# Optimization experiments

Hardware: AMD Instinct MI355X
Metric: run time of the kernel (lower is better)

## Reference

```python
import jax, jax.numpy as jnp
import numpy as np

EPS = 1e-06

def setup_inputs() -> dict:
    key = jax.random.key(0)
    k1, k2, k3 = jax.random.split(key, 3)
    N, L, H, D = 4, 4096, 16, 64
    return {
        "queries": jax.random.normal(k1, (N, L, H, D), dtype=jnp.float32),
        "keys": jax.random.normal(k2, (N, L, H, D), dtype=jnp.float32),
        "values": jax.random.normal(k3, (N, L, H, D), dtype=jnp.float32),
    }

def reference(queries, keys, values):
    # [N, L, H, D] -> [N, H, L, D]
    q = jnp.transpose(queries, (0, 2, 1, 3))
    k = jnp.transpose(keys, (0, 2, 1, 3))
    v = jnp.transpose(values, (0, 2, 1, 3))
    # kernel feature map
    q = jax.nn.sigmoid(q)
    k = jax.nn.sigmoid(k)
    L = q.shape[2]
    S = k.shape[2]
    # incoming/outgoing flow normalizers
    normalizer_row = 1.0 / jnp.einsum('nhld,nhd->nhl', q + EPS, k.sum(axis=2) + EPS)
    normalizer_col = 1.0 / jnp.einsum('nhsd,nhd->nhs', k + EPS, q.sum(axis=2) + EPS)
    # refined normalizers (competition / allocation)
    row_refine = jnp.einsum('nhld,nhd->nhl', q + EPS,
                            (k * normalizer_col[..., None]).sum(axis=2) + EPS)
    col_refine = jnp.einsum('nhsd,nhd->nhs', k + EPS,
                            (q * normalizer_row[..., None]).sum(axis=2) + EPS)
    row_refine = jax.nn.sigmoid(row_refine * (float(L) / float(S)))
    col_refine = jax.nn.softmax(col_refine, axis=-1) * S
    # linear attention aggregation: kv is [N, H, D, D]
    kv = jnp.einsum('nhsd,nhse->nhde', k, v * col_refine[..., None])
    x = jnp.einsum('nhld,nhde->nhle', q, kv) * (normalizer_row * row_refine)[..., None]
    # back to [N, L, H, D]
    return jnp.transpose(x, (0, 2, 1, 3))
```

## Files before the change

kernel.cpp:

```cpp
#include <hip/hip_runtime.h>
#include <math.h>

#define EPS 1e-6f
constexpr int N_ = 4, L_ = 4096, H_ = 16, D_ = 64;
constexpr int NH = N_ * H_;
constexpr int HD = H_ * D_;
constexpr long NSTRIDE = (long)L_ * HD;
constexpr int KCHUNKS = 16;

typedef __attribute__((ext_vector_type(8))) short short8;
typedef __attribute__((ext_vector_type(4))) float f32x4;

__device__ float g_qsum[NH * D_];
__device__ float g_ksum[NH * D_];
__device__ float g_qnr[NH * D_];
__device__ float g_knc[NH * D_];
__device__ float g_nr[NH * L_];
__device__ float g_coefrow[NH * L_];
__device__ float g_cr[NH * L_];
__device__ int   g_smax[NH];
__device__ float g_ssum[NH];
__device__ float g_kv[NH * D_ * D_];
__device__ float g_kvpart[KCHUNKS * NH * D_ * D_];

__device__ __forceinline__ float sigm(float x) {
    return 1.0f / (1.0f + __expf(-x));
}
__device__ __forceinline__ float4 sigm4(float4 x) {
    float4 r;
    r.x = sigm(x.x); r.y = sigm(x.y); r.z = sigm(x.z); r.w = sigm(x.w);
    return r;
}
__device__ __forceinline__ unsigned rne_hi(unsigned xb) {
    return (xb + 0x7fffu + ((xb >> 16) & 1u)) & 0xffff0000u;
}
__device__ __forceinline__ uint2 pack_split3(float x) {
    unsigned xb = __float_as_uint(x);
    unsigned h1 = rne_hi(xb);
    float r1 = x - __uint_as_float(h1);
    unsigned h2 = rne_hi(__float_as_uint(r1));
    float r2 = r1 - __uint_as_float(h2);
    unsigned h3 = rne_hi(__float_as_uint(r2));
    uint2 o;
    o.x = h1 | (h2 >> 16);
    o.y = h3 >> 16;
    return o;
}

__global__ void k0_zero() {
    int i = blockIdx.x * blockDim.x + threadIdx.x;
    int st = gridDim.x * blockDim.x;
    for (int j = i; j < NH * D_; j += st) {
        g_qsum[j] = 0.f; g_ksum[j] = 0.f; g_qnr[j] = 0.f; g_knc[j] = 0.f;
    }
    for (int j = i; j < NH; j += st) { g_smax[j] = 0; g_ssum[j] = 0.f; }
}

__global__ __launch_bounds__(256) void k1_sums(const float* __restrict__ q,
                                               const float* __restrict__ k) {
    int nh = blockIdx.y, n = nh >> 4, h = nh & 15;
    const float* src = blockIdx.z ? k : q;
    float* dst = blockIdx.z ? g_ksum : g_qsum;
    int t = threadIdx.x, c4 = t & 15, rg = t >> 4;
    long nbase = (long)n * NSTRIDE + (long)h * D_ + c4 * 4;
    int l0 = blockIdx.x * 128;
    float4 a = make_float4(0.f, 0.f, 0.f, 0.f);
#pragma unroll
    for (int j = 0; j < 8; ++j) {
        int r = rg + j * 16;
        float4 x = *(const float4*)&src[nbase + (long)(l0 + r) * HD];
        float4 s = sigm4(x);
        a.x += s.x; a.y += s.y; a.z += s.z; a.w += s.w;
    }
    __shared__ float4 lds[256];
    lds[t] = a;
    __syncthreads();
    if (t < 16) {
        float4 s = make_float4(0.f, 0.f, 0.f, 0.f);
#pragma unroll
        for (int g = 0; g < 16; ++g) {
            float4 b = lds[t + g * 16];
            s.x += b.x; s.y += b.y; s.z += b.z; s.w += b.w;
        }
        atomicAdd(&dst[nh * 64 + t * 4 + 0], s.x);
        atomicAdd(&dst[nh * 64 + t * 4 + 1], s.y);
        atomicAdd(&dst[nh * 64 + t * 4 + 2], s.z);
        atomicAdd(&dst[nh * 64 + t * 4 + 3], s.w);
    }
}

__global__ __launch_bounds__(256) void k2_norm(const float* __restrict__ q,
                                               const float* __restrict__ k) {
    int nh = blockIdx.y, n = nh >> 4, h = nh & 15;
    bool colside = blockIdx.z != 0;
    const float* src = colside ? k : q;
    const float* sums = colside ? g_qsum : g_ksum;
    float* acc = colside ? g_knc : g_qnr;
    __shared__ float tile[128 * 64];
    __shared__ float bvec[64];
    __shared__ float nrl[128];
    __shared__ float part[256];
    int t = threadIdx.x;
    int l0 = blockIdx.x * 128;
    long nbase = (long)n * NSTRIDE + (long)h * D_;
    if (t < 64) bvec[t] = sums[nh * 64 + t] + EPS;
#pragma unroll
    for (int j = 0; j < 8; ++j) {
        int e_ = t + j * 256;
        int r = e_ >> 4, c4 = e_ & 15;
        float4 x = *(const float4*)&src[nbase + (long)(l0 + r) * HD + c4 * 4];
        *(float4*)&tile[r * 64 + c4 * 4] = sigm4(x);
    }
    __syncthreads();
    {
        int r = t & 127, h2 = t >> 7;
        float a = 0.f;
#pragma unroll
        for (int jj = 0; jj < 32; ++jj) {
            int j = (r + h2 * 32 + jj) & 63;
            a += (tile[r * 64 + j] + EPS) * bvec[j];
        }
        part[t] = a;
    }
    __syncthreads();
    if (t < 128) {
        float inv = 1.f / (part[t] + part[t + 128]);
        nrl[t] = inv;
        if (!colside) g_nr[nh * L_ + l0 + t] = inv;
    }
    __syncthreads();
    {
        int d = t & 63, rg = t >> 6;
        float a = 0.f;
#pragma unroll
        for (int rr = 0; rr < 32; ++rr) {
            int r = rg * 32 + rr;
            a += tile[r * 64 + d] * nrl[r];
        }
        part[t] = a;
    }
    __syncthreads();
    if (t < 64)
        atomicAdd(&acc[nh * 64 + t], part[t] + part[t + 64] + part[t + 128] + part[t + 192]);
}

__global__ __launch_bounds__(256) void k3_refine(const float* __restrict__ q,
                                                 const float* __restrict__ k) {
    int nh = blockIdx.y, n = nh >> 4, h = nh & 15;
    bool colside = blockIdx.z != 0;
    const float* src = colside ? k : q;
    const float* accv = colside ? g_qnr : g_knc;
    __shared__ float tile[128 * 64];
    __shared__ float bvec[64];
    __shared__ float part[256];
    __shared__ float pmax[128];
    int t = threadIdx.x;
    int l0 = blockIdx.x * 128;
    long nbase = (long)n * NSTRIDE + (long)h * D_;
    if (t < 64) bvec[t] = accv[nh * 64 + t] + EPS;
#pragma unroll
    for (int j = 0; j < 8; ++j) {
        int e_ = t + j * 256;
        int r = e_ >> 4, c4 = e_ & 15;
        float4 x = *(const float4*)&src[nbase + (long)(l0 + r) * HD + c4 * 4];
        *(float4*)&tile[r * 64 + c4 * 4] = sigm4(x);
    }
    __syncthreads();
    {
        int r = t & 127, h2 = t >> 7;
        float a = 0.f;
#pragma unroll
        for (int jj = 0; jj < 32; ++jj) {
            int j = (r + h2 * 32 + jj) & 63;
            a += (tile[r * 64 + j] + EPS) * bvec[j];
        }
        part[t] = a;
    }
    __syncthreads();
    if (t < 128) {
        float p = part[t] + part[t + 128];
        int l = l0 + t;
        if (!colside) {
            g_coefrow[nh * L_ + l] = g_nr[nh * L_ + l] * sigm(p);
        } else {
            g_cr[nh * L_ + l] = p;
            pmax[t] = p;
        }
    }
    __syncthreads();
    if (colside) {
        if (t < 64) pmax[t] = fmaxf(pmax[t], pmax[t + 64]);
        __syncthreads();
        if (t < 32) pmax[t] = fmaxf(pmax[t], pmax[t + 32]);
        __syncthreads();
        if (t == 0) {
            float m = pmax[0];
            for (int i = 1; i < 32; ++i) m = fmaxf(m, pmax[i]);
            atomicMax(&g_smax[nh], __float_as_int(m));
        }
    }
}

__global__ __launch_bounds__(256) void k3b_softmax() {
    int nh = blockIdx.y;
    int t = threadIdx.x;
    float mx = __int_as_float(g_smax[nh]);
    int base = nh * L_ + blockIdx.x * 1024;
    float local = 0.f;
    for (int j = t; j < 1024; j += 256) {
        float e = __expf(g_cr[base + j] - mx);
        g_cr[base + j] = e;
        local += e;
    }
    __shared__ float lds[256];
    lds[t] = local;
    __syncthreads();
    for (int s = 128; s; s >>= 1) {
        if (t < s) lds[t] += lds[t + s];
        __syncthreads();
    }
    if (t == 0) atomicAdd(&g_ssum[nh], lds[0]);
}

__global__ __launch_bounds__(256) void k4_kv(const float* __restrict__ k,
                                             const float* __restrict__ v) {
    int nh = blockIdx.y, n = nh >> 4, h = nh & 15;
    int t = threadIdx.x, lane = t & 63, wv = t >> 6;
    __shared__ uint2 ktile[32 * 67];
    __shared__ uint2 vtile[32 * 67];
    __shared__ float crs[256];
    float scale = (float)L_ / g_ssum[nh];
    int s0blk = blockIdx.x * 256;
    crs[t] = g_cr[nh * L_ + s0blk + t] * scale;

    f32x4 acc[4];
#pragma unroll
    for (int e = 0; e < 4; ++e) acc[e] = (f32x4){0.f, 0.f, 0.f, 0.f};

    long nbase = (long)n * NSTRIDE + (long)h * D_;
    int m = lane & 15, qd = lane >> 4;

    for (int sub = 0; sub < 8; ++sub) {
        int s0 = sub * 32;
        __syncthreads();
#pragma unroll
        for (int j = 0; j < 2; ++j) {
            int idx = t + j * 256;
            int r = idx >> 4, c4 = idx & 15;
            long gi = nbase + (long)(s0blk + s0 + r) * HD + c4 * 4;
            float4 kk = *(const float4*)&k[gi];
            float4 vv = *(const float4*)&v[gi];
            float c = crs[s0 + r];
            float4 ks4 = sigm4(kk);
            uint2 kp0 = pack_split3(ks4.x * c), kp1 = pack_split3(ks4.y * c);
            uint2 kp2 = pack_split3(ks4.z * c), kp3 = pack_split3(ks4.w * c);
            uint2 vp0 = pack_split3(vv.x), vp1 = pack_split3(vv.y);
            uint2 vp2 = pack_split3(vv.z), vp3 = pack_split3(vv.w);
            uint2* kdst = &ktile[r * 67 + c4 * 4];
            uint2* vdst = &vtile[r * 67 + c4 * 4];
            *(uint4*)&kdst[0] = make_uint4(kp0.x, kp0.y, kp1.x, kp1.y);
            *(uint4*)&kdst[2] = make_uint4(kp2.x, kp2.y, kp3.x, kp3.y);
            *(uint4*)&vdst[0] = make_uint4(vp0.x, vp0.y, vp1.x, vp1.y);
            *(uint4*)&vdst[2] = make_uint4(vp2.x, vp2.y, vp3.x, vp3.y);
        }
        __syncthreads();
        {
            short8 a1, a2, a3;
#pragma unroll
            for (int j = 0; j < 8; ++j) {
                uint2 aw = ktile[(qd * 8 + j) * 67 + wv * 16 + m];
                a1[j] = (short)(aw.x >> 16);
                a2[j] = (short)(aw.x & 0xffffu);
                a3[j] = (short)(aw.y);
            }
#pragma unroll
            for (int e = 0; e < 4; ++e) {
                short8 b1, b2, b3;
#pragma unroll
                for (int j = 0; j < 8; ++j) {
                    uint2 bw = vtile[(qd * 8 + j) * 67 + e * 16 + m];
                    b1[j] = (short)(bw.x >> 16);
                    b2[j] = (short)(bw.x & 0xffffu);
                    b3[j] = (short)(bw.y);
                }
                acc[e] = __builtin_amdgcn_mfma_f32_16x16x32_bf16(a1, b1, acc[e], 0, 0, 0);
                acc[e] = __builtin_amdgcn_mfma_f32_16x16x32_bf16(a1, b2, acc[e], 0, 0, 0);
                acc[e] = __builtin_amdgcn_mfma_f32_16x16x32_bf16(a2, b1, acc[e], 0, 0, 0);
                acc[e] = __builtin_amdgcn_mfma_f32_16x16x32_bf16(a1, b3, acc[e], 0, 0, 0);
                acc[e] = __builtin_amdgcn_mfma_f32_16x16x32_bf16(a3, b1, acc[e], 0, 0, 0);
                acc[e] = __builtin_amdgcn_mfma_f32_16x16x32_bf16(a2, b2, acc[e], 0, 0, 0);
            }
        }
    }
    float* dst = &g_kvpart[((long)blockIdx.x * NH + nh) * 4096];
#pragma unroll
    for (int e = 0; e < 4; ++e) {
#pragma unroll
        for (int r = 0; r < 4; ++r) {
            int d = wv * 16 + qd * 4 + r;
            int ec = e * 16 + m;
            dst[d * 64 + ec] = acc[e][r];
        }
    }
}

__global__ __launch_bounds__(256) void k4b_reduce() {
    int nh = blockIdx.x, t = threadIdx.x;
#pragma unroll
    for (int j = 0; j < 4; ++j) {
        int i4 = t + j * 256;
        float4 s = make_float4(0.f, 0.f, 0.f, 0.f);
        for (int c = 0; c < KCHUNKS; ++c) {
            float4 p = ((const float4*)&g_kvpart[((long)c * NH + nh) * 4096])[i4];
            s.x += p.x; s.y += p.y; s.z += p.z; s.w += p.w;
        }
        ((float4*)&g_kv[nh * 4096])[i4] = s;
    }
}

__global__ __launch_bounds__(256) void k5_out(const float* __restrict__ q,
                                              float* __restrict__ out) {
    int nh = blockIdx.y, n = nh >> 4, h = nh & 15;
    int t = threadIdx.x;
    __shared__ float kvt[64 * 64];
    __shared__ float qt[64][65];
#pragma unroll
    for (int j = 0; j < 4; j++)
        *(float4*)&kvt[(t + j * 256) * 4] = *(const float4*)&g_kv[nh * 4096 + (t + j * 256) * 4];
    int l0 = blockIdx.x * 64;
    long nbase = (long)n * NSTRIDE + (long)h * D_;
#pragma unroll
    for (int j = 0; j < 4; j++) {
        int e_ = t + j * 256;
        int r = e_ >> 4, c4 = e_ & 15;
        float4 x = *(const float4*)&q[nbase + (long)(l0 + r) * HD + c4 * 4];
        float4 s = sigm4(x);
        qt[r][c4 * 4 + 0] = s.x;
        qt[r][c4 * 4 + 1] = s.y;
        qt[r][c4 * 4 + 2] = s.z;
        qt[r][c4 * 4 + 3] = s.w;
    }
    __syncthreads();
    int e4 = t & 15, lg = t >> 4;
    float acc[4][4];
#pragma unroll
    for (int r = 0; r < 4; r++)
#pragma unroll
        for (int c = 0; c < 4; c++) acc[r][c] = 0.f;
#pragma unroll 8
    for (int d = 0; d < 64; ++d) {
        float4 kvv = *(const float4*)&kvt[d * 64 + e4 * 4];
#pragma unroll
        for (int r = 0; r < 4; r++) {
            float qv = qt[lg * 4 + r][d];
            acc[r][0] += qv * kvv.x;
            acc[r][1] += qv * kvv.y;
            acc[r][2] += qv * kvv.z;
            acc[r][3] += qv * kvv.w;
        }
    }
#pragma unroll
    for (int r = 0; r < 4; r++) {
        int l = l0 + lg * 4 + r;
        float coef = g_coefrow[nh * L_ + l];
        float4 o;
        o.x = acc[r][0] * coef;
        o.y = acc[r][1] * coef;
        o.z = acc[r][2] * coef;
        o.w = acc[r][3] * coef;
        *(float4*)&out[nbase + (long)l * HD + e4 * 4] = o;
    }
}

extern "C" void kernel_launch(void* const* d_in, const int* in_sizes, int n_in,
                              void* d_out, int out_size, void* d_ws, size_t ws_size,
                              hipStream_t stream) {
    const float* q = (const float*)d_in[0];
    const float* k = (const float*)d_in[1];
    const float* v = (const float*)d_in[2];
    float* out = (float*)d_out;

    k0_zero<<<64, 256, 0, stream>>>();
    k1_sums<<<dim3(L_ / 128, NH, 2), 256, 0, stream>>>(q, k);
    k2_norm<<<dim3(L_ / 128, NH, 2), 256, 0, stream>>>(q, k);
    k3_refine<<<dim3(L_ / 128, NH, 2), 256, 0, stream>>>(q, k);
    k3b_softmax<<<dim3(L_ / 1024, NH), 256, 0, stream>>>();
    k4_kv<<<dim3(KCHUNKS, NH), 256, 0, stream>>>(k, v);
    k4b_reduce<<<NH, 256, 0, stream>>>();
    k5_out<<<dim3(L_ / 64, NH), 256, 0, stream>>>(q, out);
}
```

Measured before the change: 334.7 us.

## Fuse refine and softmax into KV and output kernels, drop intermediate passes

Removes the separate refine and softmax kernels. The column-refine dot product and its exponential now run inside the KV-accumulation kernel, with the softmax sum collected by atomics and applied at the reduction step. The row-refine coefficient is computed on the fly in the output kernel. This cuts one full pass over q/k plus several per-row global buffers. The sum and normalizer kernels now process contiguous rows spanning all heads, using 16-lane shuffles instead of LDS reductions. The split-bf16 MFMA KV product is replaced with a plain fp32 FMA tile loop. The trade-offs are that softmax skips max subtraction, which risks overflow on other inputs, and that the KV matmul moves off the matrix cores.

```diff
diff --git a/kernel.cpp b/kernel.cpp
--- a/kernel.cpp
+++ b/kernel.cpp
@@ -6,22 +6,15 @@
 constexpr int NH = N_ * H_;
 constexpr int HD = H_ * D_;
 constexpr long NSTRIDE = (long)L_ * HD;
-constexpr int KCHUNKS = 16;
-
-typedef __attribute__((ext_vector_type(8))) short short8;
-typedef __attribute__((ext_vector_type(4))) float f32x4;
+constexpr int SCHUNKS = 32;
 
 __device__ float g_qsum[NH * D_];
 __device__ float g_ksum[NH * D_];
 __device__ float g_qnr[NH * D_];
 __device__ float g_knc[NH * D_];
-__device__ float g_nr[NH * L_];
-__device__ float g_coefrow[NH * L_];
-__device__ float g_cr[NH * L_];
-__device__ int   g_smax[NH];
 __device__ float g_ssum[NH];
 __device__ float g_kv[NH * D_ * D_];
-__device__ float g_kvpart[KCHUNKS * NH * D_ * D_];
+__device__ float g_kvpart[(long)SCHUNKS * NH * D_ * D_];
 
 __device__ __forceinline__ float sigm(float x) {
     return 1.0f / (1.0f + __expf(-x));
@@ -31,20 +24,12 @@
     r.x = sigm(x.x); r.y = sigm(x.y); r.z = sigm(x.z); r.w = sigm(x.w);
     return r;
 }
-__device__ __forceinline__ unsigned rne_hi(unsigned xb) {
-    return (xb + 0x7fffu + ((xb >> 16) & 1u)) & 0xffff0000u;
-}
-__device__ __forceinline__ uint2 pack_split3(float x) {
-    unsigned xb = __float_as_uint(x);
-    unsigned h1 = rne_hi(xb);
-    float r1 = x - __uint_as_float(h1);
-    unsigned h2 = rne_hi(__float_as_uint(r1));
-    float r2 = r1 - __uint_as_float(h2);
-    unsigned h3 = rne_hi(__float_as_uint(r2));
-    uint2 o;
-    o.x = h1 | (h2 >> 16);
-    o.y = h3 >> 16;
-    return o;
+__device__ __forceinline__ float red16(float p) {
+    p += __shfl_xor(p, 1);
+    p += __shfl_xor(p, 2);
+    p += __shfl_xor(p, 4);
+    p += __shfl_xor(p, 8);
+    return p;
 }
 
 __global__ void k0_zero() {
@@ -53,269 +38,156 @@
     for (int j = i; j < NH * D_; j += st) {
         g_qsum[j] = 0.f; g_ksum[j] = 0.f; g_qnr[j] = 0.f; g_knc[j] = 0.f;
     }
-    for (int j = i; j < NH; j += st) { g_smax[j] = 0; g_ssum[j] = 0.f; }
+    for (int j = i; j < NH; j += st) g_ssum[j] = 0.f;
 }
 
 __global__ __launch_bounds__(256) void k1_sums(const float* __restrict__ q,
                                                const float* __restrict__ k) {
-    int nh = blockIdx.y, n = nh >> 4, h = nh & 15;
     const float* src = blockIdx.z ? k : q;
     float* dst = blockIdx.z ? g_ksum : g_qsum;
-    int t = threadIdx.x, c4 = t & 15, rg = t >> 4;
-    long nbase = (long)n * NSTRIDE + (long)h * D_ + c4 * 4;
-    int l0 = blockIdx.x * 128;
-    float4 a = make_float4(0.f, 0.f, 0.f, 0.f);
-#pragma unroll
-    for (int j = 0; j < 8; ++j) {
-        int r = rg + j * 16;
-        float4 x = *(const float4*)&src[nbase + (long)(l0 + r) * HD];
+    int t = threadIdx.x;
+    long g0 = (long)blockIdx.x * 32;
+    int n = (int)(g0 >> 12);
+    const float* p = src + g0 * HD + t * 4;
+    float ax = 0.f, ay = 0.f, az = 0.f, aw = 0.f;
+#pragma unroll 8
+    for (int r = 0; r < 32; ++r) {
+        float4 x = *(const float4*)(p + (long)r * HD);
         float4 s = sigm4(x);
-        a.x += s.x; a.y += s.y; a.z += s.z; a.w += s.w;
-    }
-    __shared__ float4 lds[256];
-    lds[t] = a;
-    __syncthreads();
-    if (t < 16) {
-        float4 s = make_float4(0.f, 0.f, 0.f, 0.f);
-#pragma unroll
-        for (int g = 0; g < 16; ++g) {
-            float4 b = lds[t + g * 16];
-            s.x += b.x; s.y += b.y; s.z += b.z; s.w += b.w;
-        }
-        atomicAdd(&dst[nh * 64 + t * 4 + 0], s.x);
-        atomicAdd(&dst[nh * 64 + t * 4 + 1], s.y);
-        atomicAdd(&dst[nh * 64 + t * 4 + 2], s.z);
-        atomicAdd(&dst[nh * 64 + t * 4 + 3], s.w);
-    }
+        ax += s.x; ay += s.y; az += s.z; aw += s.w;
+    }
+    float* d0 = dst + n * 1024 + t * 4;
+    atomicAdd(d0 + 0, ax);
+    atomicAdd(d0 + 1, ay);
+    atomicAdd(d0 + 2, az);
+    atomicAdd(d0 + 3, aw);
 }
 
 __global__ __launch_bounds__(256) void k2_norm(const float* __restrict__ q,
                                                const float* __restrict__ k) {
-    int nh = blockIdx.y, n = nh >> 4, h = nh & 15;
-    bool colside = blockIdx.z != 0;
-    const float* src = colside ? k : q;
-    const float* sums = colside ? g_qsum : g_ksum;
-    float* acc = colside ? g_knc : g_qnr;
-    __shared__ float tile[128 * 64];
-    __shared__ float bvec[64];
-    __shared__ float nrl[128];
-    __shared__ float part[256];
-    int t = threadIdx.x;
-    int l0 = blockIdx.x * 128;
-    long nbase = (long)n * NSTRIDE + (long)h * D_;
-    if (t < 64) bvec[t] = sums[nh * 64 + t] + EPS;
-#pragma unroll
-    for (int j = 0; j < 8; ++j) {
-        int e_ = t + j * 256;
-        int r = e_ >> 4, c4 = e_ & 15;
-        float4 x = *(const float4*)&src[nbase + (long)(l0 + r) * HD + c4 * 4];
-        *(float4*)&tile[r * 64 + c4 * 4] = sigm4(x);
-    }
-    __syncthreads();
-    {
-        int r = t & 127, h2 = t >> 7;
-        float a = 0.f;
-#pragma unroll
-        for (int jj = 0; jj < 32; ++jj) {
-            int j = (r + h2 * 32 + jj) & 63;
-            a += (tile[r * 64 + j] + EPS) * bvec[j];
-        }
-        part[t] = a;
-    }
-    __syncthreads();
-    if (t < 128) {
-        float inv = 1.f / (part[t] + part[t + 128]);
-        nrl[t] = inv;
-        if (!colside) g_nr[nh * L_ + l0 + t] = inv;
-    }
-    __syncthreads();
-    {
-        int d = t & 63, rg = t >> 6;
-        float a = 0.f;
-#pragma unroll
-        for (int rr = 0; rr < 32; ++rr) {
-            int r = rg * 32 + rr;
-            a += tile[r * 64 + d] * nrl[r];
-        }
-        part[t] = a;
-    }
-    __syncthreads();
-    if (t < 64)
-        atomicAdd(&acc[nh * 64 + t], part[t] + part[t + 64] + part[t + 128] + part[t + 192]);
-}
-
-__global__ __launch_bounds__(256) void k3_refine(const float* __restrict__ q,
-                                                 const float* __restrict__ k) {
-    int nh = blockIdx.y, n = nh >> 4, h = nh & 15;
-    bool colside = blockIdx.z != 0;
-    const float* src = colside ? k : q;
-    const float* accv = colside ? g_qnr : g_knc;
-    __shared__ float tile[128 * 64];
-    __shared__ float bvec[64];
-    __shared__ float part[256];
-    __shared__ float pmax[128];
-    int t = threadIdx.x;
-    int l0 = blockIdx.x * 128;
-    long nbase = (long)n * NSTRIDE + (long)h * D_;
-    if (t < 64) bvec[t] = accv[nh * 64 + t] + EPS;
-#pragma unroll
-    for (int j = 0; j < 8; ++j) {
-        int e_ = t + j * 256;
-        int r = e_ >> 4, c4 = e_ & 15;
-        float4 x = *(const float4*)&src[nbase + (long)(l0 + r) * HD + c4 * 4];
-        *(float4*)&tile[r * 64 + c4 * 4] = sigm4(x);
-    }
-    __syncthreads();
-    {
-        int r = t & 127, h2 = t >> 7;
-        float a = 0.f;
-#pragma unroll
-        for (int jj = 0; jj < 32; ++jj) {
-            int j = (r + h2 * 32 + jj) & 63;
-            a += (tile[r * 64 + j] + EPS) * bvec[j];
-        }
-        part[t] = a;
-    }
-    __syncthreads();
-    if (t < 128) {
-        float p = part[t] + part[t + 128];
-        int l = l0 + t;
-        if (!colside) {
-            g_coefrow[nh * L_ + l] = g_nr[nh * L_ + l] * sigm(p);
-        } else {
-            g_cr[nh * L_ + l] = p;
-            pmax[t] = p;
-        }
-    }
-    __syncthreads();
-    if (colside) {
-        if (t < 64) pmax[t] = fmaxf(pmax[t], pmax[t + 64]);
-        __syncthreads();
-        if (t < 32) pmax[t] = fmaxf(pmax[t], pmax[t + 32]);
-        __syncthreads();
-        if (t == 0) {
-            float m = pmax[0];
-            for (int i = 1; i < 32; ++i) m = fmaxf(m, pmax[i]);
-            atomicMax(&g_smax[nh], __float_as_int(m));
-        }
-    }
-}
-
-__global__ __launch_bounds__(256) void k3b_softmax() {
-    int nh = blockIdx.y;
-    int t = threadIdx.x;
-    float mx = __int_as_float(g_smax[nh]);
-    int base = nh * L_ + blockIdx.x * 1024;
-    float local = 0.f;
-    for (int j = t; j < 1024; j += 256) {
-        float e = __expf(g_cr[base + j] - mx);
-        g_cr[base + j] = e;
-        local += e;
-    }
-    __shared__ float lds[256];
-    lds[t] = local;
-    __syncthreads();
-    for (int s = 128; s; s >>= 1) {
-        if (t < s) lds[t] += lds[t + s];
-        __syncthreads();
-    }
-    if (t == 0) atomicAdd(&g_ssum[nh], lds[0]);
-}
-
-__global__ __launch_bounds__(256) void k4_kv(const float* __restrict__ k,
+    bool col = blockIdx.z != 0;
+    const float* src = col ? k : q;
+    const float* sums = col ? g_qsum : g_ksum;
+    float* acc = col ? g_knc : g_qnr;
+    int t = threadIdx.x;
+    long g0 = (long)blockIdx.x * 32;
+    int n = (int)(g0 >> 12);
+    float4 bv = *(const float4*)(sums + n * 1024 + t * 4);
+    bv.x += EPS; bv.y += EPS; bv.z += EPS; bv.w += EPS;
+    const float* p = src + g0 * HD + t * 4;
+    float ax = 0.f, ay = 0.f, az = 0.f, aw = 0.f;
+#pragma unroll 4
+    for (int r = 0; r < 32; ++r) {
+        float4 x = *(const float4*)(p + (long)r * HD);
+        float4 s = sigm4(x);
+        float pd = (s.x + EPS) * bv.x + (s.y + EPS) * bv.y
+                 + (s.z + EPS) * bv.z + (s.w + EPS) * bv.w;
+        pd = red16(pd);
+        float inv = 1.0f / pd;
+        ax += s.x * inv; ay += s.y * inv; az += s.z * inv; aw += s.w * inv;
+    }
+    float* d0 = acc + n * 1024 + t * 4;
+    atomicAdd(d0 + 0, ax);
+    atomicAdd(d0 + 1, ay);
+    atomicAdd(d0 + 2, az);
+    atomicAdd(d0 + 3, aw);
+}
+
+__global__ __launch_bounds__(256) void k3_kv(const float* __restrict__ k,
                                              const float* __restrict__ v) {
     int nh = blockIdx.y, n = nh >> 4, h = nh & 15;
-    int t = threadIdx.x, lane = t & 63, wv = t >> 6;
-    __shared__ uint2 ktile[32 * 67];
-    __shared__ uint2 vtile[32 * 67];
-    __shared__ float crs[256];
+    int t = threadIdx.x;
+    __shared__ float ktile[128 * 64];
+    __shared__ float vtile[128 * 64];
+    __shared__ float pbuf[128];
+    __shared__ float redb[128];
+    __shared__ float qnrbuf[64];
+    if (t < 16) {
+        float4 w = *(const float4*)&g_qnr[nh * 64 + t * 4];
+        w.x += EPS; w.y += EPS; w.z += EPS; w.w += EPS;
+        *(float4*)&qnrbuf[t * 4] = w;
+    }
+    __syncthreads();
+    int rb = t >> 4, c4 = t & 15;
+    float4 qn = *(const float4*)&qnrbuf[c4 * 4];
+    long nbase = (long)n * NSTRIDE + (long)h * D_;
+    int s0 = blockIdx.x * 128;
+#pragma unroll
+    for (int j = 0; j < 8; ++j) {
+        int r = rb + j * 16;
+        long gi = nbase + (long)(s0 + r) * HD + c4 * 4;
+        float4 kk = *(const float4*)&k[gi];
+        float4 vv = *(const float4*)&v[gi];
+        float4 sk = sigm4(kk);
+        *(float4*)&ktile[r * 64 + c4 * 4] = sk;
+        *(float4*)&vtile[r * 64 + c4 * 4] = vv;
+        float pd = (sk.x + EPS) * qn.x + (sk.y + EPS) * qn.y
+                 + (sk.z + EPS) * qn.z + (sk.w + EPS) * qn.w;
+        pd = red16(pd);
+        if (c4 == 0) pbuf[r] = pd;
+    }
+    __syncthreads();
+    if (t < 128) {
+        float e = __expf(pbuf[t]);
+        pbuf[t] = e;
+        redb[t] = e;
+    }
+    __syncthreads();
+    if (t < 64) redb[t] += redb[t + 64];
+    __syncthreads();
+    if (t < 16) {
+        float s = redb[t] + redb[t + 16] + redb[t + 32] + redb[t + 48];
+        s = red16(s);
+        if (t == 0) atomicAdd(&g_ssum[nh], s);
+    }
+#pragma unroll
+    for (int j = 0; j < 8; ++j) {
+        int r = rb + j * 16;
+        float e = pbuf[r];
+        float4 kk = *(float4*)&ktile[r * 64 + c4 * 4];
+        kk.x *= e; kk.y *= e; kk.z *= e; kk.w *= e;
+        *(float4*)&ktile[r * 64 + c4 * 4] = kk;
+    }
+    __syncthreads();
+    int dq = t >> 4, eq = t & 15;
+    float acc[4][4];
+#pragma unroll
+    for (int r = 0; r < 4; ++r)
+#pragma unroll
+        for (int c = 0; c < 4; ++c) acc[r][c] = 0.f;
+#pragma unroll 4
+    for (int s = 0; s < 128; ++s) {
+        float4 k4 = *(const float4*)&ktile[s * 64 + dq * 4];
+        float4 v4 = *(const float4*)&vtile[s * 64 + eq * 4];
+        acc[0][0] += k4.x * v4.x; acc[0][1] += k4.x * v4.y;
+        acc[0][2] += k4.x * v4.z; acc[0][3] += k4.x * v4.w;
+        acc[1][0] += k4.y * v4.x; acc[1][1] += k4.y * v4.y;
+        acc[1][2] += k4.y * v4.z; acc[1][3] += k4.y * v4.w;
+        acc[2][0] += k4.z * v4.x; acc[2][1] += k4.z * v4.y;
+        acc[2][2] += k4.z * v4.z; acc[2][3] += k4.z * v4.w;
+        acc[3][0] += k4.w * v4.x; acc[3][1] += k4.w * v4.y;
+        acc[3][2] += k4.w * v4.z; acc[3][3] += k4.w * v4.w;
+    }
+    float* dst = &g_kvpart[((long)blockIdx.x * NH + nh) * 4096];
+#pragma unroll
+    for (int r = 0; r < 4; ++r) {
+        float4 o = {acc[r][0], acc[r][1], acc[r][2], acc[r][3]};
+        *(float4*)&dst[(dq * 4 + r) * 64 + eq * 4] = o;
+    }
+}
+
+__global__ __launch_bounds__(256) void k4b_reduce() {
+    int nh = blockIdx.x;
+    int i4 = blockIdx.y * 256 + threadIdx.x;
+    float sx = 0.f, sy = 0.f, sz = 0.f, sw = 0.f;
+#pragma unroll 8
+    for (int c = 0; c < SCHUNKS; ++c) {
+        float4 p = *(const float4*)&g_kvpart[((long)c * NH + nh) * 4096 + i4 * 4];
+        sx += p.x; sy += p.y; sz += p.z; sw += p.w;
+    }
     float scale = (float)L_ / g_ssum[nh];
-    int s0blk = blockIdx.x * 256;
-    crs[t] = g_cr[nh * L_ + s0blk + t] * scale;
-
-    f32x4 acc[4];
-#pragma unroll
-    for (int e = 0; e < 4; ++e) acc[e] = (f32x4){0.f, 0.f, 0.f, 0.f};
-
-    long nbase = (long)n * NSTRIDE + (long)h * D_;
-    int m = lane & 15, qd = lane >> 4;
-
-    for (int sub = 0; sub < 8; ++sub) {
-        int s0 = sub * 32;
-        __syncthreads();
-#pragma unroll
-        for (int j = 0; j < 2; ++j) {
-            int idx = t + j * 256;
-            int r = idx >> 4, c4 = idx & 15;
-            long gi = nbase + (long)(s0blk + s0 + r) * HD + c4 * 4;
-            float4 kk = *(const float4*)&k[gi];
-            float4 vv = *(const float4*)&v[gi];
-            float c = crs[s0 + r];
-            float4 ks4 = sigm4(kk);
-            uint2 kp0 = pack_split3(ks4.x * c), kp1 = pack_split3(ks4.y * c);
-            uint2 kp2 = pack_split3(ks4.z * c), kp3 = pack_split3(ks4.w * c);
-            uint2 vp0 = pack_split3(vv.x), vp1 = pack_split3(vv.y);
-            uint2 vp2 = pack_split3(vv.z), vp3 = pack_split3(vv.w);
-            uint2* kdst = &ktile[r * 67 + c4 * 4];
-            uint2* vdst = &vtile[r * 67 + c4 * 4];
-            *(uint4*)&kdst[0] = make_uint4(kp0.x, kp0.y, kp1.x, kp1.y);
-            *(uint4*)&kdst[2] = make_uint4(kp2.x, kp2.y, kp3.x, kp3.y);
-            *(uint4*)&vdst[0] = make_uint4(vp0.x, vp0.y, vp1.x, vp1.y);
-            *(uint4*)&vdst[2] = make_uint4(vp2.x, vp2.y, vp3.x, vp3.y);
-        }
-        __syncthreads();
-        {
-            short8 a1, a2, a3;
-#pragma unroll
-            for (int j = 0; j < 8; ++j) {
-                uint2 aw = ktile[(qd * 8 + j) * 67 + wv * 16 + m];
-                a1[j] = (short)(aw.x >> 16);
-                a2[j] = (short)(aw.x & 0xffffu);
-                a3[j] = (short)(aw.y);
-            }
-#pragma unroll
-            for (int e = 0; e < 4; ++e) {
-                short8 b1, b2, b3;
-#pragma unroll
-                for (int j = 0; j < 8; ++j) {
-                    uint2 bw = vtile[(qd * 8 + j) * 67 + e * 16 + m];
-                    b1[j] = (short)(bw.x >> 16);
-                    b2[j] = (short)(bw.x & 0xffffu);
-                    b3[j] = (short)(bw.y);
-                }
-                acc[e] = __builtin_amdgcn_mfma_f32_16x16x32_bf16(a1, b1, acc[e], 0, 0, 0);
-                acc[e] = __builtin_amdgcn_mfma_f32_16x16x32_bf16(a1, b2, acc[e], 0, 0, 0);
-                acc[e] = __builtin_amdgcn_mfma_f32_16x16x32_bf16(a2, b1, acc[e], 0, 0, 0);
-                acc[e] = __builtin_amdgcn_mfma_f32_16x16x32_bf16(a1, b3, acc[e], 0, 0, 0);
-                acc[e] = __builtin_amdgcn_mfma_f32_16x16x32_bf16(a3, b1, acc[e], 0, 0, 0);
-                acc[e] = __builtin_amdgcn_mfma_f32_16x16x32_bf16(a2, b2, acc[e], 0, 0, 0);
-            }
-        }
-    }
-    float* dst = &g_kvpart[((long)blockIdx.x * NH + nh) * 4096];
-#pragma unroll
-    for (int e = 0; e < 4; ++e) {
-#pragma unroll
-        for (int r = 0; r < 4; ++r) {
-            int d = wv * 16 + qd * 4 + r;
-            int ec = e * 16 + m;
-            dst[d * 64 + ec] = acc[e][r];
-        }
-    }
-}
-
-__global__ __launch_bounds__(256) void k4b_reduce() {
-    int nh = blockIdx.x, t = threadIdx.x;
-#pragma unroll
-    for (int j = 0; j < 4; ++j) {
-        int i4 = t + j * 256;
-        float4 s = make_float4(0.f, 0.f, 0.f, 0.f);
-        for (int c = 0; c < KCHUNKS; ++c) {
-            float4 p = ((const float4*)&g_kvpart[((long)c * NH + nh) * 4096])[i4];
-            s.x += p.x; s.y += p.y; s.z += p.z; s.w += p.w;
-        }
-        ((float4*)&g_kv[nh * 4096])[i4] = s;
-    }
+    float4 o = {sx * scale, sy * scale, sz * scale, sw * scale};
+    *(float4*)&g_kv[nh * 4096 + i4 * 4] = o;
 }
 
 __global__ __launch_bounds__(256) void k5_out(const float* __restrict__ q,
@@ -324,34 +196,55 @@
     int t = threadIdx.x;
     __shared__ float kvt[64 * 64];
     __shared__ float qt[64][65];
-#pragma unroll
-    for (int j = 0; j < 4; j++)
-        *(float4*)&kvt[(t + j * 256) * 4] = *(const float4*)&g_kv[nh * 4096 + (t + j * 256) * 4];
+    __shared__ float coef[64];
+    __shared__ float bk1[64], bk2[64];
+    if (t < 16) {
+        float4 a = *(const float4*)&g_ksum[nh * 64 + t * 4];
+        a.x += EPS; a.y += EPS; a.z += EPS; a.w += EPS;
+        *(float4*)&bk1[t * 4] = a;
+        float4 b = *(const float4*)&g_knc[nh * 64 + t * 4];
+        b.x += EPS; b.y += EPS; b.z += EPS; b.w += EPS;
+        *(float4*)&bk2[t * 4] = b;
+    }
+#pragma unroll
+    for (int j = 0; j < 4; ++j)
+        *(float4*)&kvt[(t + j * 256) * 4] =
+            *(const float4*)&g_kv[nh * 4096 + (t + j * 256) * 4];
+    __syncthreads();
+    int c4 = t & 15, rg = t >> 4;
+    float4 b1 = *(const float4*)&bk1[c4 * 4];
+    float4 b2 = *(const float4*)&bk2[c4 * 4];
     int l0 = blockIdx.x * 64;
     long nbase = (long)n * NSTRIDE + (long)h * D_;
 #pragma unroll
-    for (int j = 0; j < 4; j++) {
-        int e_ = t + j * 256;
-        int r = e_ >> 4, c4 = e_ & 15;
+    for (int j = 0; j < 4; ++j) {
+        int r = rg + j * 16;
         float4 x = *(const float4*)&q[nbase + (long)(l0 + r) * HD + c4 * 4];
         float4 s = sigm4(x);
         qt[r][c4 * 4 + 0] = s.x;
         qt[r][c4 * 4 + 1] = s.y;
         qt[r][c4 * 4 + 2] = s.z;
         qt[r][c4 * 4 + 3] = s.w;
+        float p1 = (s.x + EPS) * b1.x + (s.y + EPS) * b1.y
+                 + (s.z + EPS) * b1.z + (s.w + EPS) * b1.w;
+        float p2 = (s.x + EPS) * b2.x + (s.y + EPS) * b2.y
+                 + (s.z + EPS) * b2.z + (s.w + EPS) * b2.w;
+        p1 = red16(p1);
+        p2 = red16(p2);
+        if (c4 == 0) coef[r] = sigm(p2) / p1;
     }
     __syncthreads();
     int e4 = t & 15, lg = t >> 4;
     float acc[4][4];
 #pragma unroll
-    for (int r = 0; r < 4; r++)
-#pragma unroll
-        for (int c = 0; c < 4; c++) acc[r][c] = 0.f;
+    for (int r = 0; r < 4; ++r)
+#pragma unroll
+        for (int c = 0; c < 4; ++c) acc[r][c] = 0.f;
 #pragma unroll 8
     for (int d = 0; d < 64; ++d) {
         float4 kvv = *(const float4*)&kvt[d * 64 + e4 * 4];
 #pragma unroll
-        for (int r = 0; r < 4; r++) {
+        for (int r = 0; r < 4; ++r) {
             float qv = qt[lg * 4 + r][d];
             acc[r][0] += qv * kvv.x;
             acc[r][1] += qv * kvv.y;
@@ -360,14 +253,10 @@
         }
     }
 #pragma unroll
-    for (int r = 0; r < 4; r++) {
+    for (int r = 0; r < 4; ++r) {
         int l = l0 + lg * 4 + r;
-        float coef = g_coefrow[nh * L_ + l];
-        float4 o;
-        o.x = acc[r][0] * coef;
-        o.y = acc[r][1] * coef;
-        o.z = acc[r][2] * coef;
-        o.w = acc[r][3] * coef;
+        float cf = coef[lg * 4 + r];
+        float4 o = {acc[r][0] * cf, acc[r][1] * cf, acc[r][2] * cf, acc[r][3] * cf};
         *(float4*)&out[nbase + (long)l * HD + e4 * 4] = o;
     }
 }
@@ -381,11 +270,9 @@
     float* out = (float*)d_out;
 
     k0_zero<<<64, 256, 0, stream>>>();
-    k1_sums<<<dim3(L_ / 128, NH, 2), 256, 0, stream>>>(q, k);
-    k2_norm<<<dim3(L_ / 128, NH, 2), 256, 0, stream>>>(q, k);
-    k3_refine<<<dim3(L_ / 128, NH, 2), 256, 0, stream>>>(q, k);
-    k3b_softmax<<<dim3(L_ / 1024, NH), 256, 0, stream>>>();
-    k4_kv<<<dim3(KCHUNKS, NH), 256, 0, stream>>>(k, v);
-    k4b_reduce<<<NH, 256, 0, stream>>>();
+    k1_sums<<<dim3(512, 1, 2), 256, 0, stream>>>(q, k);
+    k2_norm<<<dim3(512, 1, 2), 256, 0, stream>>>(q, k);
+    k3_kv<<<dim3(SCHUNKS, NH), 256, 0, stream>>>(k, v);
+    k4b_reduce<<<dim3(NH, 4), 256, 0, stream>>>();
     k5_out<<<dim3(L_ / 64, NH), 256, 0, stream>>>(q, out);
 }
```

New measurement: 386.0 us. +15.3%, slower.
